# Kernel tuning notes

Hardware: AMD Instinct MI355X
Metric: run time of the kernel (lower is better)

## Reference

```python
import jax, jax.numpy as jnp
import numpy as np

B, S, D = 2, 2048, 4096
H, KV, HD = 32, 8, 128          # n_heads, n_kv_heads, head_dim
N_REP = H // KV                  # GQA repeat factor
THETA = 500000.0


def setup_inputs() -> dict:
    key = jax.random.key(0)
    ks = jax.random.split(key, 5)
    x = jax.random.normal(ks[0], (B, S, D), jnp.float32)
    wq = jax.random.normal(ks[1], (D, H * HD), jnp.float32) * (D ** -0.5)
    wk = jax.random.normal(ks[2], (D, KV * HD), jnp.float32) * (D ** -0.5)
    wv = jax.random.normal(ks[3], (D, KV * HD), jnp.float32) * (D ** -0.5)
    wo = jax.random.normal(ks[4], (H * HD, D), jnp.float32) * ((H * HD) ** -0.5)
    # precomputed rotary frequencies (cos/sin of freqs_cis = exp(i * pos * inv_freq))
    inv_freq = 1.0 / (THETA ** (jnp.arange(0, HD, 2, dtype=jnp.float32) / HD))
    ang = jnp.arange(S, dtype=jnp.float32)[:, None] * inv_freq[None, :]  # [S, HD/2]
    freqs_cos = jnp.cos(ang)
    freqs_sin = jnp.sin(ang)
    # causal additive mask (prefill, start_pos=0)
    mask = jnp.triu(jnp.full((S, S), -1e9, jnp.float32), k=1)
    return dict(x=x, freqs_cos=freqs_cos, freqs_sin=freqs_sin, mask=mask,
                wq=wq, wk=wk, wv=wv, wo=wo, start_pos=0)


def _rope(t, cos, sin):
    # t: [B, S, nh, HD]; complex-pair rotation on interleaved (even, odd) channels
    tr = t.reshape(*t.shape[:-1], HD // 2, 2)
    te, to = tr[..., 0], tr[..., 1]
    c = cos[None, :, None, :]
    s = sin[None, :, None, :]
    out = jnp.stack([te * c - to * s, te * s + to * c], axis=-1)
    return out.reshape(t.shape)


def reference(x, freqs_cos, freqs_sin, mask, wq, wk, wv, wo, start_pos):
    q = (x @ wq).reshape(B, S, H, HD)
    k = (x @ wk).reshape(B, S, KV, HD)
    v = (x @ wv).reshape(B, S, KV, HD)
    q = _rope(q, freqs_cos, freqs_sin)
    k = _rope(k, freqs_cos, freqs_sin)
    # prefill: cache[:, :start_pos+S] == (k, v) since start_pos == 0
    # GQA: group query heads over KV heads instead of materializing repeat_kv
    qg = q.reshape(B, S, KV, N_REP, HD)
    scores = jnp.einsum('bqgrd,bkgd->bgrqk', qg, k) / jnp.sqrt(jnp.float32(HD))
    scores = scores + mask  # broadcast [S,S] additive causal mask
    probs = jax.nn.softmax(scores.astype(jnp.float32), axis=-1).astype(q.dtype)
    out = jnp.einsum('bgrqk,bkgd->bqgrd', probs, v).reshape(B, S, H * HD)
    return out @ wo
```

## Files before the change

kernel.cpp:

```cpp
#include <hip/hip_runtime.h>

typedef unsigned short u16;
typedef unsigned int u32;

typedef __bf16 bf16x8 __attribute__((ext_vector_type(8)));
typedef float f32x4 __attribute__((ext_vector_type(4)));

#define SEQ 2048
#define NH 32
#define NKV 8
#define HDIM 128
#define KB 32
#define QKVW 6144
#define KCOL 4096
#define VCOL 5120

__device__ __forceinline__ float b2f(u16 u) {
    return __uint_as_float(((u32)u) << 16);
}
__device__ __forceinline__ u16 f2bf(float f) {
    u32 u = __float_as_uint(f);
    u += 0x7fff + ((u >> 16) & 1);
    return (u16)(u >> 16);
}

#define GLDS16(g, l)                                                            \
    __builtin_amdgcn_global_load_lds(                                           \
        (const __attribute__((address_space(1))) void*)(g),                     \
        (__attribute__((address_space(3))) void*)(l), 16, 0, 0)

__global__ __launch_bounds__(1024) void transcvt_k(const float* __restrict__ in,
                                                   u16* __restrict__ out,
                                                   int K, int N) {
    __shared__ float tile[32][33];
    int n0 = blockIdx.x * 32, k0 = blockIdx.y * 32;
    tile[threadIdx.y][threadIdx.x] = in[(size_t)(k0 + threadIdx.y) * N + n0 + threadIdx.x];
    __syncthreads();
    out[(size_t)(n0 + threadIdx.y) * K + k0 + threadIdx.x] = f2bf(tile[threadIdx.x][threadIdx.y]);
}

__global__ __launch_bounds__(256) void cvt_k(const float* __restrict__ in,
                                             u16* __restrict__ out) {
    size_t i = ((size_t)blockIdx.x * 256 + threadIdx.x) * 8;
    float4 f0 = *(const float4*)(in + i);
    float4 f1 = *(const float4*)(in + i + 4);
    union { uint4 u4; u16 h[8]; } pk;
    pk.h[0] = f2bf(f0.x); pk.h[1] = f2bf(f0.y);
    pk.h[2] = f2bf(f0.z); pk.h[3] = f2bf(f0.w);
    pk.h[4] = f2bf(f1.x); pk.h[5] = f2bf(f1.y);
    pk.h[6] = f2bf(f1.z); pk.h[7] = f2bf(f1.w);
    *(uint4*)(out + i) = pk.u4;
}

template <bool OUT_F32>
__global__ __launch_bounds__(512, 2) void gemm256(const u16* __restrict__ A,
                                                  const u16* __restrict__ BT,
                                                  void* __restrict__ Cv,
                                                  int M, int N, int K) {
    __shared__ __align__(16) char L[131072];
    const int t = threadIdx.x, lane = t & 63, w = t >> 6;
    const int wr = w >> 2, wc = w & 3;
    const int m0 = blockIdx.y * 256, n0 = blockIdx.x * 256;
    const int r16 = lane & 15;
    const int woff = w * 1024;
    const int w8l = w * 8 + (lane >> 3);
    const int cswz = ((lane & 7) ^ (lane >> 3)) * 8;
    const u16* sA = A + (size_t)(m0 + w8l) * K + cswz;
    const u16* sB = BT + (size_t)(n0 + w8l) * K + cswz;

    const int acol0 = ((lane >> 4) * 16) ^ ((lane & 7) << 4);
    const int acol1 = (((lane >> 4) * 16) + 64) ^ ((lane & 7) << 4);
    const char* arowp = L + (wr * 128 + r16) * 128;
    const char* browp = L + 32768 + (wc * 64 + r16) * 128;

    f32x4 acc[8][4] = {};
    bf16x8 a[4][2], b0[2][2], b1[2][2];

    auto stage = [&](int bufi, int isB, int h, int kt) {
        const u16* s = isB ? sB : sA;
        char* d = (char*)L + bufi * 65536 + isB * 32768 + h * 16384 + woff;
        GLDS16(s + (size_t)(h * 128) * K + kt, d);
        GLDS16(s + (size_t)(h * 128 + 64) * K + kt, d + 8192);
    };

    const int NT = K >> 6;
    stage(0, 0, 0, 0); stage(0, 0, 1, 0); stage(0, 1, 0, 0); stage(0, 1, 1, 0);
    if (NT > 1) {
        stage(1, 0, 0, 64);
        asm volatile("s_waitcnt vmcnt(2)" ::: "memory");
    } else {
        asm volatile("s_waitcnt vmcnt(0)" ::: "memory");
    }
    __builtin_amdgcn_s_barrier();
    __builtin_amdgcn_sched_barrier(0);

    for (int T = 0; T < NT; ++T) {
        const int buf = T & 1;
        const char* Ab = arowp + buf * 65536;
        const char* Bb = browp + buf * 65536;
        const int ktn = (T + 1) << 6, ktn2 = (T + 2) << 6;

#pragma unroll
        for (int mi = 0; mi < 4; ++mi) {
            a[mi][0] = *(const bf16x8*)(Ab + mi * 2048 + acol0);
            a[mi][1] = *(const bf16x8*)(Ab + mi * 2048 + acol1);
        }
#pragma unroll
        for (int ni = 0; ni < 2; ++ni) {
            b0[ni][0] = *(const bf16x8*)(Bb + ni * 2048 + acol0);
            b0[ni][1] = *(const bf16x8*)(Bb + ni * 2048 + acol1);
        }
        if (T + 1 < NT) stage(buf ^ 1, 0, 1, ktn);
        __builtin_amdgcn_s_barrier();
        __builtin_amdgcn_sched_barrier(0);
        asm volatile("s_waitcnt lgkmcnt(0)" ::: "memory");
        __builtin_amdgcn_s_setprio(1);
#pragma unroll
        for (int mi = 0; mi < 4; ++mi)
#pragma unroll
            for (int ni = 0; ni < 2; ++ni) {
                acc[mi][ni] = __builtin_amdgcn_mfma_f32_16x16x32_bf16(a[mi][0], b0[ni][0], acc[mi][ni], 0, 0, 0);
                acc[mi][ni] = __builtin_amdgcn_mfma_f32_16x16x32_bf16(a[mi][1], b0[ni][1], acc[mi][ni], 0, 0, 0);
            }
        __builtin_amdgcn_s_setprio(0);
        __builtin_amdgcn_s_barrier();
        __builtin_amdgcn_sched_barrier(0);

#pragma unroll
        for (int ni = 0; ni < 2; ++ni) {
            b1[ni][0] = *(const bf16x8*)(Bb + (ni + 2) * 2048 + acol0);
            b1[ni][1] = *(const bf16x8*)(Bb + (ni + 2) * 2048 + acol1);
        }
        if (T + 1 < NT) stage(buf ^ 1, 1, 0, ktn);
        __builtin_amdgcn_s_barrier();
        __builtin_amdgcn_sched_barrier(0);
        asm volatile("s_waitcnt lgkmcnt(0)" ::: "memory");
        __builtin_amdgcn_s_setprio(1);
#pragma unroll
        for (int mi = 0; mi < 4; ++mi)
#pragma unroll
            for (int ni = 0; ni < 2; ++ni) {
                acc[mi][ni + 2] = __builtin_amdgcn_mfma_f32_16x16x32_bf16(a[mi][0], b1[ni][0], acc[mi][ni + 2], 0, 0, 0);
                acc[mi][ni + 2] = __builtin_amdgcn_mfma_f32_16x16x32_bf16(a[mi][1], b1[ni][1], acc[mi][ni + 2], 0, 0, 0);
            }
        __builtin_amdgcn_s_setprio(0);
        __builtin_amdgcn_s_barrier();
        __builtin_amdgcn_sched_barrier(0);

#pragma unroll
        for (int mi = 0; mi < 4; ++mi) {
            a[mi][0] = *(const bf16x8*)(Ab + (mi + 4) * 2048 + acol0);
            a[mi][1] = *(const bf16x8*)(Ab + (mi + 4) * 2048 + acol1);
        }
        if (T + 1 < NT) stage(buf ^ 1, 1, 1, ktn);
        __builtin_amdgcn_s_barrier();
        __builtin_amdgcn_sched_barrier(0);
        asm volatile("s_waitcnt lgkmcnt(0)" ::: "memory");
        __builtin_amdgcn_s_setprio(1);
#pragma unroll
        for (int mi = 0; mi < 4; ++mi)
#pragma unroll
            for (int ni = 0; ni < 2; ++ni) {
                acc[mi + 4][ni] = __builtin_amdgcn_mfma_f32_16x16x32_bf16(a[mi][0], b0[ni][0], acc[mi + 4][ni], 0, 0, 0);
                acc[mi + 4][ni] = __builtin_amdgcn_mfma_f32_16x16x32_bf16(a[mi][1], b0[ni][1], acc[mi + 4][ni], 0, 0, 0);
            }
        __builtin_amdgcn_s_setprio(0);
        __builtin_amdgcn_s_barrier();
        __builtin_amdgcn_sched_barrier(0);

        if (T + 2 < NT) stage(buf, 0, 0, ktn2);
        __builtin_amdgcn_s_setprio(1);
#pragma unroll
        for (int mi = 0; mi < 4; ++mi)
#pragma unroll
            for (int ni = 0; ni < 2; ++ni) {
                acc[mi + 4][ni + 2] = __builtin_amdgcn_mfma_f32_16x16x32_bf16(a[mi][0], b1[ni][0], acc[mi + 4][ni + 2], 0, 0, 0);
                acc[mi + 4][ni + 2] = __builtin_amdgcn_mfma_f32_16x16x32_bf16(a[mi][1], b1[ni][1], acc[mi + 4][ni + 2], 0, 0, 0);
            }
        __builtin_amdgcn_s_setprio(0);
        if (T + 2 < NT) asm volatile("s_waitcnt vmcnt(2)" ::: "memory");
        else            asm volatile("s_waitcnt vmcnt(0)" ::: "memory");
        __builtin_amdgcn_s_barrier();
        __builtin_amdgcn_sched_barrier(0);
    }

    const int r0 = (lane >> 4) * 4;
#pragma unroll
    for (int mi = 0; mi < 8; ++mi) {
#pragma unroll
        for (int r = 0; r < 4; ++r) {
            size_t row = (size_t)(m0 + wr * 128 + mi * 16 + r0 + r) * N + n0 + wc * 64;
#pragma unroll
            for (int ni = 0; ni < 4; ++ni) {
                if constexpr (OUT_F32)
                    ((float*)Cv)[row + ni * 16 + r16] = acc[mi][ni][r];
                else
                    ((u16*)Cv)[row + ni * 16 + r16] = f2bf(acc[mi][ni][r]);
            }
        }
    }
}

__global__ __launch_bounds__(256) void rope_k(u16* __restrict__ T, int col0,
                                              const float* __restrict__ cosb,
                                              const float* __restrict__ sinb,
                                              int nh) {
    int i = blockIdx.x * 256 + threadIdx.x;
    int p = i & 63;
    int h = (i >> 6) % nh;
    int bs = i / (64 * nh);
    int s = bs & (SEQ - 1);
    size_t base = (size_t)bs * QKVW + col0 + h * HDIM + 2 * p;
    ushort2 v = *(ushort2*)(T + base);
    float te = b2f(v.x), to = b2f(v.y);
    float c = cosb[s * 64 + p], sn = sinb[s * 64 + p];
    ushort2 o;
    o.x = f2bf(te * c - to * sn);
    o.y = f2bf(te * sn + to * c);
    *(ushort2*)(T + base) = o;
}

__global__ __launch_bounds__(1024) void vtrans_k(const u16* __restrict__ QKV,
                                                 u16* __restrict__ VtG) {
    __shared__ u16 tile[32][33];
    int s0 = blockIdx.x * 32, d0 = blockIdx.y * 32, plane = blockIdx.z;
    int b = plane >> 3, g = plane & 7;
    tile[threadIdx.y][threadIdx.x] =
        QKV[(size_t)(b * SEQ + s0 + threadIdx.y) * QKVW + VCOL + g * HDIM + d0 + threadIdx.x];
    __syncthreads();
    VtG[((size_t)plane * HDIM + d0 + threadIdx.y) * SEQ + s0 + threadIdx.x] =
        tile[threadIdx.x][threadIdx.y];
}

__global__ __launch_bounds__(256) void fattn_k(const u16* __restrict__ QKV,
                                               const u16* __restrict__ VtG,
                                               u16* __restrict__ O) {
    __shared__ __align__(16) u16 Ks[KB][136];
    __shared__ __align__(16) u16 Vt[HDIM][40];
    __shared__ __align__(16) u16 Ps[4][16][40];

    const int q0 = (gridDim.x - 1 - blockIdx.x) * 64;
    const int h = blockIdx.y, b = blockIdx.z;
    const int g = h >> 2;
    const int t = threadIdx.x, lane = t & 63, w = t >> 6;
    const int row16 = lane & 15, q8 = (lane >> 4) * 8, q84 = (lane >> 4) * 4;
    const float scale = 0.08838834764831845f;

    bf16x8 qf[4];
    {
        const u16* qptr = QKV + (size_t)(b * SEQ + q0 + w * 16 + row16) * QKVW + h * HDIM;
        for (int c = 0; c < 4; ++c) qf[c] = *(const bf16x8*)(qptr + c * 32 + q8);
    }

    f32x4 o[8];
    for (int c = 0; c < 8; ++c) o[c] = (f32x4){0.f, 0.f, 0.f, 0.f};
    float lsum[4] = {0.f, 0.f, 0.f, 0.f};

    const u16* kbase = QKV + (size_t)b * SEQ * QKVW + KCOL + g * HDIM;
    const u16* vtp = VtG + (size_t)(b * NKV + g) * HDIM * SEQ;

    const int ntiles = (q0 + 63) / KB + 1;
    for (int tile = 0; tile < ntiles; ++tile) {
        const int jb = tile * KB;
        __syncthreads();
        for (int i = 0; i < 2; ++i) {
            int c = t + 256 * i;
            int kr = c >> 4, kc = (c & 15) * 8;
            *(uint4*)&Ks[kr][kc] = *(const uint4*)(kbase + (size_t)(jb + kr) * QKVW + kc);
            int vr = c >> 2, vc = (c & 3) * 8;
            *(uint4*)&Vt[vr][vc] = *(const uint4*)(vtp + (size_t)vr * SEQ + jb + vc);
        }
        __syncthreads();

        for (int sub = 0; sub < 2; ++sub) {
            f32x4 sa = {0.f, 0.f, 0.f, 0.f};
            for (int c = 0; c < 4; ++c) {
                bf16x8 kf = *(const bf16x8*)&Ks[sub * 16 + row16][c * 32 + q8];
                sa = __builtin_amdgcn_mfma_f32_16x16x32_bf16(qf[c], kf, sa, 0, 0, 0);
            }
            const int kcol = jb + sub * 16 + row16;
            for (int r = 0; r < 4; ++r) {
                int qrow = q0 + w * 16 + q84 + r;
                float p = (kcol <= qrow) ? __expf(fminf(sa[r] * scale, 80.f)) : 0.f;
                lsum[r] += p;
                Ps[w][q84 + r][sub * 16 + row16] = f2bf(p);
            }
        }
        bf16x8 pf = *(const bf16x8*)&Ps[w][row16][q8];
        for (int c = 0; c < 8; ++c) {
            bf16x8 vf = *(const bf16x8*)&Vt[c * 16 + row16][q8];
            o[c] = __builtin_amdgcn_mfma_f32_16x16x32_bf16(pf, vf, o[c], 0, 0, 0);
        }
    }

    for (int r = 0; r < 4; ++r)
        for (int off = 1; off < 16; off <<= 1) lsum[r] += __shfl_xor(lsum[r], off);

    float inv[4];
    for (int r = 0; r < 4; ++r) inv[r] = 1.f / lsum[r];

    u16* optr = O + (size_t)(b * SEQ + q0 + w * 16) * (NH * HDIM) + h * HDIM;
    for (int c = 0; c < 8; ++c)
        for (int r = 0; r < 4; ++r)
            optr[(size_t)(q84 + r) * (NH * HDIM) + c * 16 + row16] = f2bf(o[c][r] * inv[r]);
}

extern "C" void kernel_launch(void* const* d_in, const int* in_sizes, int n_in,
                              void* d_out, int out_size, void* d_ws, size_t ws_size,
                              hipStream_t stream) {
    const float* x    = (const float*)d_in[0];
    const float* fcos = (const float*)d_in[1];
    const float* fsin = (const float*)d_in[2];
    const float* wq = (const float*)d_in[4];
    const float* wk = (const float*)d_in[5];
    const float* wv = (const float*)d_in[6];
    const float* wo = (const float*)d_in[7];
    float* out = (float*)d_out;

    char* wsp = (char*)d_ws;
    u16* BTall = (u16*)(wsp);
    u16* VtG   = (u16*)(wsp);
    u16* woT   = (u16*)(wsp + 50331648);
    u16* xb    = (u16*)(wsp + 83886080);
    u16* ATb   = (u16*)(wsp + 83886080);
    u16* QKVb  = (u16*)(wsp + 117440512);

    const int M = 2 * SEQ;
    const int D = 4096;
    const int NQ = NH * HDIM;

    dim3 tb(32, 32);
    transcvt_k<<<dim3(4096 / 32, D / 32), tb, 0, stream>>>(wq, BTall, D, 4096);
    transcvt_k<<<dim3(1024 / 32, D / 32), tb, 0, stream>>>(wk, BTall + (size_t)4096 * 4096, D, 1024);
    transcvt_k<<<dim3(1024 / 32, D / 32), tb, 0, stream>>>(wv, BTall + (size_t)5120 * 4096, D, 1024);
    transcvt_k<<<dim3(D / 32, NQ / 32), tb, 0, stream>>>(wo, woT, NQ, D);
    cvt_k<<<(M * D) / (256 * 8), 256, 0, stream>>>(x, xb);

    gemm256<false><<<dim3(QKVW / 256, M / 256), 512, 0, stream>>>(xb, BTall, QKVb, M, QKVW, D);

    rope_k<<<(M * NH * 64) / 256, 256, 0, stream>>>(QKVb, 0, fcos, fsin, NH);
    rope_k<<<(M * NKV * 64) / 256, 256, 0, stream>>>(QKVb, KCOL, fcos, fsin, NKV);

    vtrans_k<<<dim3(SEQ / 32, HDIM / 32, 2 * NKV), tb, 0, stream>>>(QKVb, VtG);

    fattn_k<<<dim3(SEQ / 64, NH, 2), 256, 0, stream>>>(QKVb, VtG, ATb);

    gemm256<true><<<dim3(D / 256, M / 256), 512, 0, stream>>>(ATb, woT, out, M, D, NQ);

    (void)in_sizes; (void)n_in; (void)out_size; (void)ws_size;
}
```

Measured before the change: 884.3 us.

## Double-buffer K/V tiles via async global-to-LDS loads with swizzled layout

The attention kernel now processes 64-key tiles and prefetches the next K and V^T tiles into a second LDS buffer with global_load_lds. Waits use explicit vmcnt counts, so loads overlap with the MFMA work on the current tile. The LDS layout uses an XOR swizzle to avoid bank conflicts, and s_setprio is raised around MFMA sections. The kernel now uses about 73KB of LDS per block, which lowers occupancy, and the hand-counted waitcnt logic is fragile.

```diff
diff --git a/kernel.cpp b/kernel.cpp
--- a/kernel.cpp
+++ b/kernel.cpp
@@ -10,7 +10,6 @@
 #define NH 32
 #define NKV 8
 #define HDIM 128
-#define KB 32
 #define QKVW 6144
 #define KCOL 4096
 #define VCOL 5120
@@ -235,72 +234,129 @@
 __global__ __launch_bounds__(256) void fattn_k(const u16* __restrict__ QKV,
                                                const u16* __restrict__ VtG,
                                                u16* __restrict__ O) {
-    __shared__ __align__(16) u16 Ks[KB][136];
-    __shared__ __align__(16) u16 Vt[HDIM][40];
-    __shared__ __align__(16) u16 Ps[4][16][40];
+    __shared__ __align__(16) char L[74752];
 
     const int q0 = (gridDim.x - 1 - blockIdx.x) * 64;
     const int h = blockIdx.y, b = blockIdx.z;
     const int g = h >> 2;
     const int t = threadIdx.x, lane = t & 63, w = t >> 6;
-    const int row16 = lane & 15, q8 = (lane >> 4) * 8, q84 = (lane >> 4) * 4;
+    const int row16 = lane & 15, g16 = lane >> 4;
+    const int q8 = g16 * 8, q84 = g16 * 4;
+    const int swz = (row16 & 7) << 4;
     const float scale = 0.08838834764831845f;
+
+    u16* Ps = (u16*)(L + 65536) + w * (16 * 72);
+
+    const u16* kbase = QKV + (size_t)b * SEQ * QKVW + KCOL + g * HDIM;
+    const u16* vtp = VtG + (size_t)(b * NKV + g) * HDIM * SEQ;
 
     bf16x8 qf[4];
     {
         const u16* qptr = QKV + (size_t)(b * SEQ + q0 + w * 16 + row16) * QKVW + h * HDIM;
+#pragma unroll
         for (int c = 0; c < 4; ++c) qf[c] = *(const bf16x8*)(qptr + c * 32 + q8);
     }
 
+    const int krl = lane >> 4, kch = lane & 15;
+    const int vrl = lane >> 3, vch = lane & 7;
+    auto stage = [&](int bufi, int jb) {
+#pragma unroll
+        for (int jj = 0; jj < 4; ++jj) {
+            int j = w * 4 + jj;
+            int r = j * 4 + krl;
+            int sc = kch ^ (r & 7);
+            GLDS16(kbase + (size_t)(jb + r) * QKVW + sc * 8,
+                   (char*)L + bufi * 16384 + j * 1024);
+        }
+#pragma unroll
+        for (int jj = 0; jj < 4; ++jj) {
+            int j = w * 4 + jj;
+            int r = j * 8 + vrl;
+            int sc = vch ^ (vrl & 7);
+            GLDS16(vtp + (size_t)r * SEQ + jb + sc * 8,
+                   (char*)L + 32768 + bufi * 16384 + j * 1024);
+        }
+    };
+
     f32x4 o[8];
+#pragma unroll
     for (int c = 0; c < 8; ++c) o[c] = (f32x4){0.f, 0.f, 0.f, 0.f};
     float lsum[4] = {0.f, 0.f, 0.f, 0.f};
 
-    const u16* kbase = QKV + (size_t)b * SEQ * QKVW + KCOL + g * HDIM;
-    const u16* vtp = VtG + (size_t)(b * NKV + g) * HDIM * SEQ;
-
-    const int ntiles = (q0 + 63) / KB + 1;
-    for (int tile = 0; tile < ntiles; ++tile) {
-        const int jb = tile * KB;
-        __syncthreads();
-        for (int i = 0; i < 2; ++i) {
-            int c = t + 256 * i;
-            int kr = c >> 4, kc = (c & 15) * 8;
-            *(uint4*)&Ks[kr][kc] = *(const uint4*)(kbase + (size_t)(jb + kr) * QKVW + kc);
-            int vr = c >> 2, vc = (c & 3) * 8;
-            *(uint4*)&Vt[vr][vc] = *(const uint4*)(vtp + (size_t)vr * SEQ + jb + vc);
-        }
-        __syncthreads();
-
-        for (int sub = 0; sub < 2; ++sub) {
+    const int NT = q0 / 64 + 1;
+    stage(0, 0);
+    if (NT > 1) {
+        stage(1, 64);
+        asm volatile("s_waitcnt vmcnt(8)" ::: "memory");
+    } else {
+        asm volatile("s_waitcnt vmcnt(0)" ::: "memory");
+    }
+    __builtin_amdgcn_s_barrier();
+    __builtin_amdgcn_sched_barrier(0);
+
+    for (int T = 0; T < NT; ++T) {
+        const int jb = T * 64;
+        const char* Kb = (const char*)L + (T & 1) * 16384;
+        const char* Vb = (const char*)L + 32768 + (T & 1) * 16384;
+
+#pragma unroll
+        for (int sub = 0; sub < 4; ++sub) {
             f32x4 sa = {0.f, 0.f, 0.f, 0.f};
+            const int srow = sub * 16 + row16;
+            __builtin_amdgcn_s_setprio(1);
+#pragma unroll
             for (int c = 0; c < 4; ++c) {
-                bf16x8 kf = *(const bf16x8*)&Ks[sub * 16 + row16][c * 32 + q8];
+                bf16x8 kf = *(const bf16x8*)(Kb + srow * 256 + (((c * 4 + g16) << 4) ^ swz));
                 sa = __builtin_amdgcn_mfma_f32_16x16x32_bf16(qf[c], kf, sa, 0, 0, 0);
             }
+            __builtin_amdgcn_s_setprio(0);
             const int kcol = jb + sub * 16 + row16;
+            const int qrow = q0 + w * 16 + q84;
+#pragma unroll
             for (int r = 0; r < 4; ++r) {
-                int qrow = q0 + w * 16 + q84 + r;
-                float p = (kcol <= qrow) ? __expf(fminf(sa[r] * scale, 80.f)) : 0.f;
+                float p = (kcol <= qrow + r) ? __expf(fminf(sa[r] * scale, 80.f)) : 0.f;
                 lsum[r] += p;
-                Ps[w][q84 + r][sub * 16 + row16] = f2bf(p);
-            }
-        }
-        bf16x8 pf = *(const bf16x8*)&Ps[w][row16][q8];
-        for (int c = 0; c < 8; ++c) {
-            bf16x8 vf = *(const bf16x8*)&Vt[c * 16 + row16][q8];
-            o[c] = __builtin_amdgcn_mfma_f32_16x16x32_bf16(pf, vf, o[c], 0, 0, 0);
-        }
-    }
-
+                Ps[(q84 + r) * 72 + sub * 16 + row16] = f2bf(p);
+            }
+        }
+#pragma unroll
+        for (int kk = 0; kk < 2; ++kk) {
+            bf16x8 pf = *(const bf16x8*)(Ps + row16 * 72 + kk * 32 + q8);
+            __builtin_amdgcn_s_setprio(1);
+#pragma unroll
+            for (int c = 0; c < 8; ++c) {
+                bf16x8 vf = *(const bf16x8*)(Vb + (c * 16 + row16) * 128 + (((kk * 4 + g16) << 4) ^ swz));
+                o[c] = __builtin_amdgcn_mfma_f32_16x16x32_bf16(pf, vf, o[c], 0, 0, 0);
+            }
+            __builtin_amdgcn_s_setprio(0);
+        }
+
+        if (T + 1 < NT) {
+            __builtin_amdgcn_s_barrier();
+            __builtin_amdgcn_sched_barrier(0);
+            if (T + 2 < NT) {
+                stage(T & 1, (T + 2) * 64);
+                asm volatile("s_waitcnt vmcnt(8)" ::: "memory");
+            } else {
+                asm volatile("s_waitcnt vmcnt(0)" ::: "memory");
+            }
+            __builtin_amdgcn_s_barrier();
+            __builtin_amdgcn_sched_barrier(0);
+        }
+    }
+
+#pragma unroll
     for (int r = 0; r < 4; ++r)
         for (int off = 1; off < 16; off <<= 1) lsum[r] += __shfl_xor(lsum[r], off);
 
     float inv[4];
+#pragma unroll
     for (int r = 0; r < 4; ++r) inv[r] = 1.f / lsum[r];
 
     u16* optr = O + (size_t)(b * SEQ + q0 + w * 16) * (NH * HDIM) + h * HDIM;
+#pragma unroll
     for (int c = 0; c < 8; ++c)
+#pragma unroll
         for (int r = 0; r < 4; ++r)
             optr[(size_t)(q84 + r) * (NH * HDIM) + c * 16 + row16] = f2bf(o[c][r] * inv[r]);
 }
```

Result: no change. 892.7 us (+1.0%).
